# Optimization experiments

Measured on AMD Instinct MI355X. Metric: run time of the kernel, lower is better.

## Reference

```python
import jax, jax.numpy as jnp
import numpy as np

D_MODEL = 1024
H = 16
D_K = D_MODEL // H
NEG = -1.0e9


def setup_inputs() -> dict:
    key = jax.random.key(0)
    ks = jax.random.split(key, 12)
    B, S = 2, 2048
    s = 1.0 / np.sqrt(D_MODEL)
    inp = {
        "q": jax.random.normal(ks[0], (B, S, D_MODEL), jnp.float32),
        "k": jax.random.normal(ks[1], (B, S, D_MODEL), jnp.float32),
        "v": jax.random.normal(ks[2], (B, S, D_MODEL), jnp.float32),
        "mask": jnp.tril(jnp.ones((S, S), jnp.int32))[None, None, :, :],
        "wq": jax.random.normal(ks[3], (D_MODEL, D_MODEL), jnp.float32) * s,
        "bq": jax.random.normal(ks[4], (D_MODEL,), jnp.float32) * s,
        "wk": jax.random.normal(ks[5], (D_MODEL, D_MODEL), jnp.float32) * s,
        "bk": jax.random.normal(ks[6], (D_MODEL,), jnp.float32) * s,
        "wv": jax.random.normal(ks[7], (D_MODEL, D_MODEL), jnp.float32) * s,
        "bv": jax.random.normal(ks[8], (D_MODEL,), jnp.float32) * s,
        "wo": jax.random.normal(ks[9], (D_MODEL, D_MODEL), jnp.float32) * s,
        "bo": jax.random.normal(ks[10], (D_MODEL,), jnp.float32) * s,
    }
    return inp


def _split_heads(x):
    # [B,S,D] -> [B,H,S,d_k]
    B, S, _ = x.shape
    return x.reshape(B, S, H, D_K).transpose(0, 2, 1, 3)


def reference(q, k, v, mask, wq, bq, wk, bk, wv, bv, wo, bo):
    # torch Linear: y = x @ W.T + b
    query = _split_heads(q @ wq.T + bq)
    key = _split_heads(k @ wk.T + bk)
    value = _split_heads(v @ wv.T + bv)
    # scores: [B,H,S,S]
    scores = jnp.einsum("bhqd,bhkd->bhqk", query, key) / jnp.sqrt(
        jnp.asarray(D_K, query.dtype))
    scores = jnp.where(mask == 0, jnp.asarray(NEG, scores.dtype), scores)
    attn = jax.nn.softmax(scores, axis=-1)  # dropout p=0.0 -> identity
    x = jnp.einsum("bhqk,bhkd->bhqd", attn, value)
    B, _, S, _ = x.shape
    x = x.transpose(0, 2, 1, 3).reshape(B, S, D_MODEL)
    return x @ wo.T + bo
```

## Files before the change

### kernel.cpp

```cpp
#include <hip/hip_runtime.h>
#include <hip/hip_bf16.h>
#include <cstdint>
#include <cstddef>

#define BATCH 2
#define SEQ   2048
#define DM    1024
#define NH    16
#define DK    64
#define MROWS (BATCH*SEQ)

typedef __bf16 bf16;
typedef float  f32x4  __attribute__((ext_vector_type(4)));
typedef bf16   bf16x8 __attribute__((ext_vector_type(8)));
typedef bf16   bf16x4 __attribute__((ext_vector_type(4)));

#define MFMA32(a, b, c) __builtin_amdgcn_mfma_f32_16x16x32_bf16(a, b, c, 0, 0, 0)

__device__ __forceinline__ void llds16(const void* gc, void* l) {
    void* g = (void*)gc;
    __builtin_amdgcn_global_load_lds(
        (__attribute__((address_space(1))) uint32_t*)g,
        (__attribute__((address_space(3))) uint32_t*)l,
        16, 0, 0);
}

__global__ __launch_bounds__(256) void k_convert(
    const float* __restrict__ q, const float* __restrict__ k, const float* __restrict__ v,
    const float* __restrict__ wq, const float* __restrict__ wk, const float* __restrict__ wv,
    const float* __restrict__ wo,
    bf16* __restrict__ qb, bf16* __restrict__ kb, bf16* __restrict__ vb,
    bf16* __restrict__ wqb, bf16* __restrict__ wkb, bf16* __restrict__ wvb,
    bf16* __restrict__ wob) {
    long t = (long)blockIdx.x * blockDim.x + threadIdx.x;
    const long NQ = (long)MROWS * DM / 4;
    const long NW = (long)DM * DM / 4;
    const float* src; bf16* dst; long off;
    if (t < NQ)            { src = q;  dst = qb;  off = t; }
    else if (t < 2*NQ)     { src = k;  dst = kb;  off = t - NQ; }
    else if (t < 3*NQ)     { src = v;  dst = vb;  off = t - 2*NQ; }
    else {
        long u = t - 3*NQ;
        if (u < NW)        { src = wq; dst = wqb; off = u; }
        else if (u < 2*NW) { src = wk; dst = wkb; off = u - NW; }
        else if (u < 3*NW) { src = wv; dst = wvb; off = u - 2*NW; }
        else               { src = wo; dst = wob; off = u - 3*NW; }
    }
    f32x4 x = *(const f32x4*)(src + off * 4);
    bf16x4 y;
    y[0] = (bf16)x[0]; y[1] = (bf16)x[1]; y[2] = (bf16)x[2]; y[3] = (bf16)x[3];
    *(bf16x4*)(dst + off * 4) = y;
}

__device__ __forceinline__ void gemm_main(const bf16* __restrict__ A, const bf16* __restrict__ B,
                                          int m0, int n0, f32x4 acc[4][4]) {
    constexpr int K = DM, BK = 32;
    __shared__ bf16 sA[128 * BK];
    __shared__ bf16 sB[128 * BK];
    const int tid = threadIdx.x;
    const int l = tid & 63, w = tid >> 6;
    const int quad = l >> 4, l15 = l & 15;
    const int wm = w & 1, wn = w >> 1;

    for (int k0 = 0; k0 < K; k0 += BK) {
#pragma unroll
        for (int i = 0; i < 2; ++i) {
            int r16 = w * 32 + i * 16;
            const bf16* ga = A + (size_t)(m0 + r16 + (l >> 2)) * K + k0 + (l & 3) * 8;
            const bf16* gb = B + (size_t)(n0 + r16 + (l >> 2)) * K + k0 + (l & 3) * 8;
            llds16(ga, &sA[r16 * BK]);
            llds16(gb, &sB[r16 * BK]);
        }
        __syncthreads();

        bf16x8 af[4], bfr[4];
#pragma unroll
        for (int mi = 0; mi < 4; ++mi)
            af[mi] = *(const bf16x8*)&sA[(wm * 64 + mi * 16 + l15) * BK + quad * 8];
#pragma unroll
        for (int ni = 0; ni < 4; ++ni)
            bfr[ni] = *(const bf16x8*)&sB[(wn * 64 + ni * 16 + l15) * BK + quad * 8];
#pragma unroll
        for (int mi = 0; mi < 4; ++mi)
#pragma unroll
            for (int ni = 0; ni < 4; ++ni)
                acc[mi][ni] = MFMA32(af[mi], bfr[ni], acc[mi][ni]);
        __syncthreads();
    }
}

__global__ __launch_bounds__(256) void k_gemm_qkv(
    const bf16* __restrict__ qb, const bf16* __restrict__ kb, const bf16* __restrict__ vb,
    const bf16* __restrict__ wqb, const bf16* __restrict__ wkb, const bf16* __restrict__ wvb,
    const float* __restrict__ bq, const float* __restrict__ bk, const float* __restrict__ bv,
    bf16* __restrict__ Qf, bf16* __restrict__ Kf, bf16* __restrict__ Vf) {
    const int z = blockIdx.z;
    const bf16* A; const bf16* B; const float* bias;
    int m0, n0;
    if (z == 2) {
        A = vb; B = wvb; bias = bv;
        m0 = blockIdx.x * 128;
        n0 = blockIdx.y * 128;
    } else {
        A = z ? wkb : wqb; B = z ? kb : qb; bias = z ? bk : bq;
        m0 = blockIdx.y * 128;
        n0 = blockIdx.x * 128;
    }
    f32x4 acc[4][4] = {};
    gemm_main(A, B, m0, n0, acc);

    const int tid = threadIdx.x, l = tid & 63, w = tid >> 6;
    const int quad = l >> 4, l15 = l & 15;
    const int wm = w & 1, wn = w >> 1;

    if (z == 2) {
#pragma unroll
        for (int ni = 0; ni < 4; ++ni) {
            int dcol = n0 + wn * 64 + ni * 16 + l15;
            int hh2 = dcol >> 6;
            int dtile = (dcol >> 4) & 3;
            float bias_v = bias[dcol];
#pragma unroll
            for (int mi = 0; mi < 4; ++mi) {
                int srow = m0 + wm * 64 + mi * 16;
                int bb = srow >> 11, sl = srow & 2047;
                int kc = sl >> 5;
                int qp = 2 * (mi & 1) + (quad >> 1);
                bf16x4 pack;
#pragma unroll
                for (int r = 0; r < 4; ++r)
                    pack[r] = (bf16)(acc[mi][ni][r] + bias_v);
                size_t entry = ((size_t)(bb * NH + hh2) * 64 + kc) * 4 + dtile;
                *(bf16x4*)(Vf + entry * 512 + (size_t)(qp * 16 + l15) * 8 + (quad & 1) * 4) = pack;
            }
        }
    } else {
        bf16* out = z ? Kf : Qf;
        const float scale = z ? 1.0f : 0.18033688f;
        float bias_rv[4][4];
#pragma unroll
        for (int mi = 0; mi < 4; ++mi)
#pragma unroll
            for (int r = 0; r < 4; ++r)
                bias_rv[mi][r] = bias[m0 + wm * 64 + mi * 16 + quad * 4 + r];
#pragma unroll
        for (int ni = 0; ni < 4; ++ni) {
            int scol = n0 + wn * 64 + ni * 16 + l15;
            int bb = scol >> 11, s = scol & 2047;
            int s16 = s >> 4;
#pragma unroll
            for (int mi = 0; mi < 4; ++mi) {
                int drow = m0 + wm * 64 + mi * 16;
                int hh2 = (drow >> 6) & 15;
                int chunk = (drow & 63) >> 5;
                int qp = 2 * (mi & 1) + (quad >> 1);
                bf16x4 pack;
#pragma unroll
                for (int r = 0; r < 4; ++r)
                    pack[r] = (bf16)((acc[mi][ni][r] + bias_rv[mi][r]) * scale);
                size_t entry = ((size_t)(bb * NH + hh2) * 128 + s16) * 2 + chunk;
                *(bf16x4*)(out + entry * 512 + (size_t)(qp * 16 + l15) * 8 + (quad & 1) * 4) = pack;
            }
        }
    }
}

__global__ __launch_bounds__(256) void k_gemm_out(
    const bf16* __restrict__ X, const bf16* __restrict__ wob,
    const float* __restrict__ bo, float* __restrict__ out) {
    constexpr int K = DM, BK = 32;
    const int m0 = blockIdx.y * 128, n0 = blockIdx.x * 64;
    __shared__ bf16 sA[128 * BK];
    __shared__ bf16 sB[64 * BK];
    const int tid = threadIdx.x;
    const int l = tid & 63, w = tid >> 6;
    const int quad = l >> 4, l15 = l & 15;
    const int wm = w & 1, wn = w >> 1;

    f32x4 acc[4][2] = {};
    for (int k0 = 0; k0 < K; k0 += BK) {
#pragma unroll
        for (int i = 0; i < 2; ++i) {
            int r16 = w * 32 + i * 16;
            const bf16* ga = X + (size_t)(m0 + r16 + (l >> 2)) * K + k0 + (l & 3) * 8;
            llds16(ga, &sA[r16 * BK]);
        }
        {
            int r16 = w * 16;
            const bf16* gb = wob + (size_t)(n0 + r16 + (l >> 2)) * K + k0 + (l & 3) * 8;
            llds16(gb, &sB[r16 * BK]);
        }
        __syncthreads();

        bf16x8 af[4], bfr[2];
#pragma unroll
        for (int mi = 0; mi < 4; ++mi)
            af[mi] = *(const bf16x8*)&sA[(wm * 64 + mi * 16 + l15) * BK + quad * 8];
#pragma unroll
        for (int ni = 0; ni < 2; ++ni)
            bfr[ni] = *(const bf16x8*)&sB[(wn * 32 + ni * 16 + l15) * BK + quad * 8];
#pragma unroll
        for (int mi = 0; mi < 4; ++mi)
#pragma unroll
            for (int ni = 0; ni < 2; ++ni)
                acc[mi][ni] = MFMA32(af[mi], bfr[ni], acc[mi][ni]);
        __syncthreads();
    }
#pragma unroll
    for (int mi = 0; mi < 4; ++mi)
#pragma unroll
        for (int ni = 0; ni < 2; ++ni) {
            int col = n0 + wn * 32 + ni * 16 + l15;
            float bias_v = bo[col];
            int rbase = m0 + wm * 64 + mi * 16 + quad * 4;
#pragma unroll
            for (int r = 0; r < 4; ++r)
                out[(size_t)(rbase + r) * DM + col] = acc[mi][ni][r] + bias_v;
        }
}

__global__ __launch_bounds__(128, 3) void k_flash(const bf16* __restrict__ Qf,
                                                  const bf16* __restrict__ Kf,
                                                  const bf16* __restrict__ Vf,
                                                  bf16* __restrict__ X) {
    const int bh = blockIdx.x;
    const int qt32 = 63 - ((blockIdx.y + bh) & 63);
    const int b = bh >> 4, h = bh & 15;
    const int tid = threadIdx.x, w = tid >> 6, l = tid & 63;
    const int quad = l >> 4, l15 = l & 15;
    __shared__ bf16 P[2][16 * 72];
    bf16* Pw = P[w];

    const int qt16 = qt32 * 2 + w;
    const bf16* qfp = Qf + (size_t)bh * 128 * 1024;
    const bf16* kfp = Kf + (size_t)bh * 128 * 1024;
    const bf16* vfp = Vf + (size_t)bh * 64 * 4 * 512;

    bf16x8 qf[2];
#pragma unroll
    for (int c = 0; c < 2; ++c)
        qf[c] = *(const bf16x8*)(qfp + ((size_t)qt16 * 2 + c) * 512 + (size_t)l * 8);

    f32x4 o[4] = {};
    float lp = 0.f;
    const int jmax = qt16 >> 2;
    const int qglob = qt16 * 16 + l15;

    for (int j = 0; j <= jmax; ++j) {
        bf16x8 kl[4][2];
#pragma unroll
        for (int ni = 0; ni < 4; ++ni)
#pragma unroll
            for (int c = 0; c < 2; ++c)
                kl[ni][c] = *(const bf16x8*)(kfp + ((size_t)(j * 4 + ni) * 2 + c) * 512 + (size_t)l * 8);

        f32x4 st[4];
#pragma unroll
        for (int ni = 0; ni < 4; ++ni) {
            f32x4 zz = {};
            zz = MFMA32(kl[ni][0], qf[0], zz);
            st[ni] = MFMA32(kl[ni][1], qf[1], zz);
        }

        bf16x8 vl[2][4];
#pragma unroll
        for (int c = 0; c < 2; ++c)
#pragma unroll
            for (int dt = 0; dt < 4; ++dt)
                vl[c][dt] = *(const bf16x8*)(vfp + ((size_t)(j * 2 + c) * 4 + dt) * 512 + (size_t)l * 8);

        const bool diag = (j == jmax);
#pragma unroll
        for (int ni = 0; ni < 4; ++ni) {
            bf16x4 ev;
#pragma unroll
            for (int r = 0; r < 4; ++r) {
                float s = st[ni][r];
                if (diag) {
                    int key = j * 64 + ni * 16 + quad * 4 + r;
                    if (key > qglob) s = -1e30f;
                }
                float e = __builtin_amdgcn_exp2f(s);
                lp += e;
                ev[r] = (bf16)e;
            }
            *(bf16x4*)&Pw[l15 * 72 + ni * 16 + quad * 4] = ev;
        }

#pragma unroll
        for (int c = 0; c < 2; ++c) {
            bf16x8 pb = *(const bf16x8*)&Pw[l15 * 72 + c * 32 + quad * 8];
#pragma unroll
            for (int dt = 0; dt < 4; ++dt)
                o[dt] = MFMA32(vl[c][dt], pb, o[dt]);
        }
    }

    lp += __shfl_xor(lp, 16, 64);
    lp += __shfl_xor(lp, 32, 64);
    float rv = 1.f / lp;

#pragma unroll
    for (int dt = 0; dt < 4; ++dt) {
        bf16x4 pk;
#pragma unroll
        for (int r = 0; r < 4; ++r)
            pk[r] = (bf16)(o[dt][r] * rv);
        *(bf16x4*)&Pw[l15 * 72 + dt * 16 + quad * 4] = pk;
    }
#pragma unroll
    for (int i = 0; i < 2; ++i) {
        int row = i * 8 + (l >> 3);
        bf16x8 vv = *(const bf16x8*)&Pw[row * 72 + (l & 7) * 8];
        *(bf16x8*)(X + (size_t)(b * SEQ + qt16 * 16 + row) * DM + h * 64 + (l & 7) * 8) = vv;
    }
}

extern "C" void kernel_launch(void* const* d_in, const int* in_sizes, int n_in,
                              void* d_out, int out_size, void* d_ws, size_t ws_size,
                              hipStream_t stream) {
    const float* q  = (const float*)d_in[0];
    const float* k  = (const float*)d_in[1];
    const float* v  = (const float*)d_in[2];
    const float* wq = (const float*)d_in[4];
    const float* bq = (const float*)d_in[5];
    const float* wk = (const float*)d_in[6];
    const float* bk = (const float*)d_in[7];
    const float* wv = (const float*)d_in[8];
    const float* bv = (const float*)d_in[9];
    const float* wo = (const float*)d_in[10];
    const float* bo = (const float*)d_in[11];
    float* out = (float*)d_out;

    uint8_t* ws = (uint8_t*)d_ws;
    const size_t SZ_ACT = (size_t)MROWS * DM * sizeof(bf16);
    const size_t SZ_W   = (size_t)DM * DM * sizeof(bf16);
    bf16* qb  = (bf16*)(ws);
    bf16* kb  = (bf16*)(ws + SZ_ACT);
    bf16* vb  = (bf16*)(ws + 2 * SZ_ACT);
    bf16* wqb = (bf16*)(ws + 3 * SZ_ACT);
    bf16* wkb = (bf16*)(ws + 3 * SZ_ACT + SZ_W);
    bf16* wvb = (bf16*)(ws + 3 * SZ_ACT + 2 * SZ_W);
    bf16* wob = (bf16*)(ws + 3 * SZ_ACT + 3 * SZ_W);
    bf16* Qf  = (bf16*)(ws + 3 * SZ_ACT + 4 * SZ_W);
    bf16* Kf  = (bf16*)(ws + 4 * SZ_ACT + 4 * SZ_W);
    bf16* Vf  = (bf16*)(ws + 5 * SZ_ACT + 4 * SZ_W);
    bf16* X   = (bf16*)(ws + 6 * SZ_ACT + 4 * SZ_W);

    {
        long total_vec4 = 3L * MROWS * DM / 4 + 4L * DM * DM / 4;
        k_convert<<<dim3((unsigned)(total_vec4 / 256)), 256, 0, stream>>>(
            q, k, v, wq, wk, wv, wo, qb, kb, vb, wqb, wkb, wvb, wob);
    }
    k_gemm_qkv<<<dim3(32, 8, 3), 256, 0, stream>>>(
        qb, kb, vb, wqb, wkb, wvb, bq, bk, bv, Qf, Kf, Vf);
    k_flash<<<dim3(BATCH * NH, SEQ / 32), 128, 0, stream>>>(Qf, Kf, Vf, X);
    k_gemm_out<<<dim3(DM / 64, MROWS / 128), 256, 0, stream>>>(X, wob, bo, out);
}
```

Before: 238.5 us.

## Share K/V tiles via LDS across 4 waves and double GEMM K-step

The flash kernel moves to 256-thread blocks covering 64 query rows. K and V tiles are staged into shared memory with direct global-to-LDS loads, so four waves reuse one copy instead of each wave reading them from global memory. The block ordering over query tiles is also simplified. Both GEMMs raise BK to 64 and lay shared memory out as contiguous 16x32 fragment tiles, which removes the strided LDS indexing and halves the number of barrier iterations. The cost is two barriers per key tile in attention and a coarser causal grid that may balance load less evenly.

New measurement: 250.6 us. 1.05x slower.

```diff
diff --git a/kernel.cpp b/kernel.cpp
--- a/kernel.cpp
+++ b/kernel.cpp
@@ -54,37 +54,41 @@
 
 __device__ __forceinline__ void gemm_main(const bf16* __restrict__ A, const bf16* __restrict__ B,
                                           int m0, int n0, f32x4 acc[4][4]) {
-    constexpr int K = DM, BK = 32;
-    __shared__ bf16 sA[128 * BK];
-    __shared__ bf16 sB[128 * BK];
+    constexpr int K = DM, BK = 64;
+    __shared__ bf16 sA[16 * 512];
+    __shared__ bf16 sB[16 * 512];
     const int tid = threadIdx.x;
     const int l = tid & 63, w = tid >> 6;
-    const int quad = l >> 4, l15 = l & 15;
+    const int lr = l & 15, lc = l >> 4;
     const int wm = w & 1, wn = w >> 1;
 
     for (int k0 = 0; k0 < K; k0 += BK) {
 #pragma unroll
-        for (int i = 0; i < 2; ++i) {
-            int r16 = w * 32 + i * 16;
-            const bf16* ga = A + (size_t)(m0 + r16 + (l >> 2)) * K + k0 + (l & 3) * 8;
-            const bf16* gb = B + (size_t)(n0 + r16 + (l >> 2)) * K + k0 + (l & 3) * 8;
-            llds16(ga, &sA[r16 * BK]);
-            llds16(gb, &sB[r16 * BK]);
-        }
-        __syncthreads();
-
-        bf16x8 af[4], bfr[4];
-#pragma unroll
-        for (int mi = 0; mi < 4; ++mi)
-            af[mi] = *(const bf16x8*)&sA[(wm * 64 + mi * 16 + l15) * BK + quad * 8];
-#pragma unroll
-        for (int ni = 0; ni < 4; ++ni)
-            bfr[ni] = *(const bf16x8*)&sB[(wn * 64 + ni * 16 + l15) * BK + quad * 8];
-#pragma unroll
-        for (int mi = 0; mi < 4; ++mi)
+        for (int i = 0; i < 4; ++i) {
+            int e = w * 4 + i;
+            int kc = e >> 3, t16 = e & 7;
+            const bf16* ga = A + (size_t)(m0 + t16 * 16 + lr) * K + k0 + kc * 32 + lc * 8;
+            const bf16* gb = B + (size_t)(n0 + t16 * 16 + lr) * K + k0 + kc * 32 + lc * 8;
+            llds16(ga, &sA[e * 512]);
+            llds16(gb, &sB[e * 512]);
+        }
+        __syncthreads();
+
+#pragma unroll
+        for (int kk = 0; kk < 2; ++kk) {
+            bf16x8 af[4], bfr[4];
+#pragma unroll
+            for (int mi = 0; mi < 4; ++mi)
+                af[mi] = *(const bf16x8*)&sA[(size_t)(kk * 8 + wm * 4 + mi) * 512 + l * 8];
 #pragma unroll
             for (int ni = 0; ni < 4; ++ni)
-                acc[mi][ni] = MFMA32(af[mi], bfr[ni], acc[mi][ni]);
+                bfr[ni] = *(const bf16x8*)&sB[(size_t)(kk * 8 + wn * 4 + ni) * 512 + l * 8];
+#pragma unroll
+            for (int mi = 0; mi < 4; ++mi)
+#pragma unroll
+                for (int ni = 0; ni < 4; ++ni)
+                    acc[mi][ni] = MFMA32(af[mi], bfr[ni], acc[mi][ni]);
+        }
         __syncthreads();
     }
 }
@@ -168,42 +172,47 @@
 __global__ __launch_bounds__(256) void k_gemm_out(
     const bf16* __restrict__ X, const bf16* __restrict__ wob,
     const float* __restrict__ bo, float* __restrict__ out) {
-    constexpr int K = DM, BK = 32;
+    constexpr int K = DM, BK = 64;
     const int m0 = blockIdx.y * 128, n0 = blockIdx.x * 64;
-    __shared__ bf16 sA[128 * BK];
-    __shared__ bf16 sB[64 * BK];
+    __shared__ bf16 sA[16 * 512];
+    __shared__ bf16 sB[8 * 512];
     const int tid = threadIdx.x;
     const int l = tid & 63, w = tid >> 6;
+    const int lr = l & 15, lc = l >> 4;
     const int quad = l >> 4, l15 = l & 15;
     const int wm = w & 1, wn = w >> 1;
 
     f32x4 acc[4][2] = {};
     for (int k0 = 0; k0 < K; k0 += BK) {
 #pragma unroll
+        for (int i = 0; i < 4; ++i) {
+            int e = w * 4 + i;
+            int kc = e >> 3, mt = e & 7;
+            llds16(X + (size_t)(m0 + mt * 16 + lr) * K + k0 + kc * 32 + lc * 8, &sA[e * 512]);
+        }
+#pragma unroll
         for (int i = 0; i < 2; ++i) {
-            int r16 = w * 32 + i * 16;
-            const bf16* ga = X + (size_t)(m0 + r16 + (l >> 2)) * K + k0 + (l & 3) * 8;
-            llds16(ga, &sA[r16 * BK]);
-        }
-        {
-            int r16 = w * 16;
-            const bf16* gb = wob + (size_t)(n0 + r16 + (l >> 2)) * K + k0 + (l & 3) * 8;
-            llds16(gb, &sB[r16 * BK]);
-        }
-        __syncthreads();
-
-        bf16x8 af[4], bfr[2];
-#pragma unroll
-        for (int mi = 0; mi < 4; ++mi)
-            af[mi] = *(const bf16x8*)&sA[(wm * 64 + mi * 16 + l15) * BK + quad * 8];
-#pragma unroll
-        for (int ni = 0; ni < 2; ++ni)
-            bfr[ni] = *(const bf16x8*)&sB[(wn * 32 + ni * 16 + l15) * BK + quad * 8];
-#pragma unroll
-        for (int mi = 0; mi < 4; ++mi)
+            int e = w * 2 + i;
+            int kc = e >> 2, nt = e & 3;
+            llds16(wob + (size_t)(n0 + nt * 16 + lr) * K + k0 + kc * 32 + lc * 8, &sB[e * 512]);
+        }
+        __syncthreads();
+
+#pragma unroll
+        for (int kk = 0; kk < 2; ++kk) {
+            bf16x8 af[4], bfr[2];
+#pragma unroll
+            for (int mi = 0; mi < 4; ++mi)
+                af[mi] = *(const bf16x8*)&sA[(size_t)(kk * 8 + wm * 4 + mi) * 512 + l * 8];
 #pragma unroll
             for (int ni = 0; ni < 2; ++ni)
-                acc[mi][ni] = MFMA32(af[mi], bfr[ni], acc[mi][ni]);
+                bfr[ni] = *(const bf16x8*)&sB[(size_t)(kk * 4 + wn * 2 + ni) * 512 + l * 8];
+#pragma unroll
+            for (int mi = 0; mi < 4; ++mi)
+#pragma unroll
+                for (int ni = 0; ni < 2; ++ni)
+                    acc[mi][ni] = MFMA32(af[mi], bfr[ni], acc[mi][ni]);
+        }
         __syncthreads();
     }
 #pragma unroll
@@ -219,23 +228,27 @@
         }
 }
 
-__global__ __launch_bounds__(128, 3) void k_flash(const bf16* __restrict__ Qf,
+__global__ __launch_bounds__(256, 4) void k_flash(const bf16* __restrict__ Qf,
                                                   const bf16* __restrict__ Kf,
                                                   const bf16* __restrict__ Vf,
                                                   bf16* __restrict__ X) {
     const int bh = blockIdx.x;
-    const int qt32 = 63 - ((blockIdx.y + bh) & 63);
+    const int qt = 31 - (int)blockIdx.y;
     const int b = bh >> 4, h = bh & 15;
     const int tid = threadIdx.x, w = tid >> 6, l = tid & 63;
     const int quad = l >> 4, l15 = l & 15;
-    __shared__ bf16 P[2][16 * 72];
+    __shared__ bf16 sK[8 * 512];
+    __shared__ bf16 sV[8 * 512];
+    __shared__ bf16 P[4][16 * 72];
     bf16* Pw = P[w];
 
-    const int qt16 = qt32 * 2 + w;
     const bf16* qfp = Qf + (size_t)bh * 128 * 1024;
     const bf16* kfp = Kf + (size_t)bh * 128 * 1024;
     const bf16* vfp = Vf + (size_t)bh * 64 * 4 * 512;
 
+    const int qt16 = qt * 4 + w;
+    const int qglob = qt16 * 16 + l15;
+
     bf16x8 qf[2];
 #pragma unroll
     for (int c = 0; c < 2; ++c)
@@ -243,33 +256,27 @@
 
     f32x4 o[4] = {};
     float lp = 0.f;
-    const int jmax = qt16 >> 2;
-    const int qglob = qt16 * 16 + l15;
-
-    for (int j = 0; j <= jmax; ++j) {
-        bf16x8 kl[4][2];
-#pragma unroll
-        for (int ni = 0; ni < 4; ++ni)
-#pragma unroll
-            for (int c = 0; c < 2; ++c)
-                kl[ni][c] = *(const bf16x8*)(kfp + ((size_t)(j * 4 + ni) * 2 + c) * 512 + (size_t)l * 8);
+
+    for (int j = 0; j <= qt; ++j) {
+#pragma unroll
+        for (int i = 0; i < 2; ++i) {
+            int e = w * 2 + i;
+            llds16(kfp + ((size_t)(j * 8 + e)) * 512 + (size_t)l * 8, &sK[e * 512]);
+            llds16(vfp + ((size_t)(j * 8 + e)) * 512 + (size_t)l * 8, &sV[e * 512]);
+        }
+        __syncthreads();
 
         f32x4 st[4];
 #pragma unroll
         for (int ni = 0; ni < 4; ++ni) {
+            bf16x8 k0 = *(const bf16x8*)&sK[(size_t)(ni * 2 + 0) * 512 + l * 8];
+            bf16x8 k1 = *(const bf16x8*)&sK[(size_t)(ni * 2 + 1) * 512 + l * 8];
             f32x4 zz = {};
-            zz = MFMA32(kl[ni][0], qf[0], zz);
-            st[ni] = MFMA32(kl[ni][1], qf[1], zz);
-        }
-
-        bf16x8 vl[2][4];
-#pragma unroll
-        for (int c = 0; c < 2; ++c)
-#pragma unroll
-            for (int dt = 0; dt < 4; ++dt)
-                vl[c][dt] = *(const bf16x8*)(vfp + ((size_t)(j * 2 + c) * 4 + dt) * 512 + (size_t)l * 8);
-
-        const bool diag = (j == jmax);
+            zz = MFMA32(k0, qf[0], zz);
+            st[ni] = MFMA32(k1, qf[1], zz);
+        }
+
+        const bool diag = (j == qt);
 #pragma unroll
         for (int ni = 0; ni < 4; ++ni) {
             bf16x4 ev;
@@ -291,9 +298,12 @@
         for (int c = 0; c < 2; ++c) {
             bf16x8 pb = *(const bf16x8*)&Pw[l15 * 72 + c * 32 + quad * 8];
 #pragma unroll
-            for (int dt = 0; dt < 4; ++dt)
-                o[dt] = MFMA32(vl[c][dt], pb, o[dt]);
-        }
+            for (int dt = 0; dt < 4; ++dt) {
+                bf16x8 vv = *(const bf16x8*)&sV[(size_t)(c * 4 + dt) * 512 + l * 8];
+                o[dt] = MFMA32(vv, pb, o[dt]);
+            }
+        }
+        __syncthreads();
     }
 
     lp += __shfl_xor(lp, 16, 64);
@@ -354,6 +364,6 @@
     }
     k_gemm_qkv<<<dim3(32, 8, 3), 256, 0, stream>>>(
         qb, kb, vb, wqb, wkb, wvb, bq, bk, bv, Qf, Kf, Vf);
-    k_flash<<<dim3(BATCH * NH, SEQ / 32), 128, 0, stream>>>(Qf, Kf, Vf, X);
+    k_flash<<<dim3(BATCH * NH, SEQ / 64), 256, 0, stream>>>(Qf, Kf, Vf, X);
     k_gemm_out<<<dim3(DM / 64, MROWS / 128), 256, 0, stream>>>(X, wob, bo, out);
 }
```
